# Kernel tuning notes

Hardware: AMD Instinct MI355X
Metric: run time of the kernel (lower is better)

The kernel has to match this reference:

```python
import jax, jax.numpy as jnp
import numpy as np

B, T, N, F_IN, H, E, L = 4, 12, 10000, 16, 64, 160000, 2


def setup_inputs() -> dict:
    key = jax.random.key(0)
    ks = jax.random.split(key, 10)
    s = 0.05  # small init scale for stability
    return {
        "x": jax.random.normal(ks[0], (B, T, N, F_IN), jnp.float32),
        "edge_index": jax.random.randint(ks[1], (2, E), 0, N, dtype=jnp.int32),
        "edge_weight": jax.random.uniform(ks[2], (E,), jnp.float32),
        "W_pre": jax.random.normal(ks[3], (F_IN, H), jnp.float32) * s,
        "b_pre": jnp.zeros((H,), jnp.float32),
        "W_lin": jax.random.normal(ks[4], (L, H, H), jnp.float32) * s,
        "W_root": jax.random.normal(ks[5], (L, H, H), jnp.float32) * s,
        "b_conv": jnp.zeros((L, H), jnp.float32),
        "W_ih": jax.random.normal(ks[6], (3 * H, H), jnp.float32) * s,
        "W_hh": jax.random.normal(ks[7], (3 * H, H), jnp.float32) * s,
        "b_ih": jnp.zeros((3 * H,), jnp.float32),
        "b_hh": jnp.zeros((3 * H,), jnp.float32),
    }


def reference(x, edge_index, edge_weight, W_pre, b_pre, W_lin, W_root, b_conv,
              W_ih, W_hh, b_ih, b_hh):
    b, t, n, _ = x.shape
    hdim = W_pre.shape[1]

    # preprocess: LazyLinear + ReLU, then fold time into batch: (b*t, n, h)
    h = jax.nn.relu(x @ W_pre + b_pre).reshape(b * t, n, hdim)

    # symmetric edge normalization (GCN-style): w_ij / sqrt(deg_i * deg_j)
    src, dst = edge_index[0], edge_index[1]
    deg = jnp.zeros((n,), h.dtype).at[dst].add(edge_weight)
    dinv = jnp.where(deg > 0, jax.lax.rsqrt(jnp.where(deg > 0, deg, 1.0)), 0.0)
    w = dinv[src] * edge_weight * dinv[dst]  # [E]

    # stacked GraphConv layers: gather -> weight -> scatter-add + root + bias, ReLU
    for l in range(W_lin.shape[0]):
        m = h @ W_lin[l]                                   # [BT, N, H]
        msg = m[:, src, :] * w[None, :, None]              # [BT, E, H] gather
        agg = jnp.zeros_like(m).at[:, dst, :].add(msg)     # scatter-add
        h = jax.nn.relu(agg + h @ W_root[l] + b_conv[l])

    # (b, t, n, h) -> (b*n, t, h) sequences for the GRU
    seq = h.reshape(b, t, n, hdim).transpose(0, 2, 1, 3).reshape(b * n, t, hdim)

    def gru_step(hprev, xt):
        gi = xt @ W_ih.T + b_ih
        gh = hprev @ W_hh.T + b_hh
        i_r, i_z, i_n = jnp.split(gi, 3, axis=-1)
        h_r, h_z, h_n = jnp.split(gh, 3, axis=-1)
        r = jax.nn.sigmoid(i_r + h_r)
        z = jax.nn.sigmoid(i_z + h_z)
        ng = jnp.tanh(i_n + r * h_n)
        hnew = (1.0 - z) * ng + z * hprev
        return hnew, None

    h0 = jnp.zeros((b * n, hdim), h.dtype)
    hlast, _ = jax.lax.scan(gru_step, h0, seq.transpose(1, 0, 2))  # carry = last output
    return hlast.reshape(b, n, hdim)
```

## Files before the change

### kernel.cpp

```cpp
#include <hip/hip_runtime.h>
#include <cstdint>
#include <cstddef>

#define B_ 4
#define T_ 12
#define N_ 10000
#define FIN_ 16
#define H_ 64
#define E_ 160000
#define BT_ (B_*T_)
#define ROWS_ (BT_*N_)
#define GRU_ROWS_ (B_*N_)
#define PAD_ 68

__device__ __forceinline__ float sigmoidf_(float x){ return 1.0f/(1.0f + __expf(-x)); }
__device__ __forceinline__ float tanhf_(float x){
  float ax = fabsf(x);
  float e  = __expf(-2.0f*ax);
  float t  = (1.0f - e)/(1.0f + e);
  return copysignf(t, x);
}

__global__ __launch_bounds__(256) void k_pre(const float* __restrict__ x,
    const float* __restrict__ Wp, const float* __restrict__ bp,
    float* __restrict__ A){
  __shared__ float sW[FIN_*H_];
  __shared__ float sb[H_];
  for (int i = threadIdx.x; i < FIN_*H_; i += 256) sW[i] = Wp[i];
  if (threadIdx.x < H_) sb[threadIdx.x] = bp[threadIdx.x];
  __syncthreads();
  int r = blockIdx.x*256 + threadIdx.x;
  if (r >= ROWS_) return;
  int bt = r / N_;
  int n  = r - bt*N_;
  const float4* xr = reinterpret_cast<const float4*>(x + (size_t)r*FIN_);
  float4 xv[4];
  #pragma unroll
  for (int i=0;i<4;i++) xv[i] = xr[i];
  const float* xk = reinterpret_cast<const float*>(xv);
  float4 acc[16];
  #pragma unroll
  for (int j=0;j<16;j++) acc[j] = reinterpret_cast<const float4*>(sb)[j];
  #pragma unroll
  for (int k=0;k<16;k++){
    float a = xk[k];
    const float4* wr = reinterpret_cast<const float4*>(sW + k*H_);
    #pragma unroll
    for (int j=0;j<16;j++){
      float4 w = wr[j];
      acc[j].x = fmaf(a, w.x, acc[j].x);
      acc[j].y = fmaf(a, w.y, acc[j].y);
      acc[j].z = fmaf(a, w.z, acc[j].z);
      acc[j].w = fmaf(a, w.w, acc[j].w);
    }
  }
  float4* outp = reinterpret_cast<float4*>(A + ((size_t)n*BT_ + bt)*H_);
  #pragma unroll
  for (int j=0;j<16;j++){
    float4 o = acc[j];
    o.x = fmaxf(o.x, 0.f); o.y = fmaxf(o.y, 0.f);
    o.z = fmaxf(o.z, 0.f); o.w = fmaxf(o.w, 0.f);
    outp[j] = o;
  }
}

__global__ void k_deg(const int* __restrict__ ei, const float* __restrict__ ew,
                      float* __restrict__ wdeg, int* __restrict__ cnt){
  int e = blockIdx.x*256 + threadIdx.x;
  if (e >= E_) return;
  int d = ei[E_ + e];
  atomicAdd(&wdeg[d], ew[e]);
  atomicAdd(&cnt[d], 1);
}

__global__ __launch_bounds__(1024) void k_scan(const int* __restrict__ cnt,
                                               int* __restrict__ rs){
  __shared__ int sb[1024];
  int tid = threadIdx.x;
  int base = tid*10;
  int loc[10]; int s = 0;
  #pragma unroll
  for (int j=0;j<10;j++){
    loc[j] = s;
    int v = (base+j < N_) ? cnt[base+j] : 0;
    s += v;
  }
  sb[tid] = s;
  __syncthreads();
  for (int off=1; off<1024; off<<=1){
    int v = (tid >= off) ? sb[tid-off] : 0;
    __syncthreads();
    sb[tid] += v;
    __syncthreads();
  }
  int pre = (tid>0) ? sb[tid-1] : 0;
  #pragma unroll
  for (int j=0;j<10;j++){
    if (base+j <= N_) rs[base+j] = pre + loc[j];
  }
}

__global__ void k_dinv(const float* __restrict__ wdeg, float* __restrict__ dinv){
  int i = blockIdx.x*256 + threadIdx.x;
  if (i >= N_) return;
  float dg = wdeg[i];
  dinv[i] = (dg > 0.f) ? rsqrtf(dg) : 0.f;
}

__global__ void k_fill(const int* __restrict__ ei, const float* __restrict__ ew,
                       const float* __restrict__ dinv, const int* __restrict__ rs,
                       int* __restrict__ fillc, int* __restrict__ src_s,
                       float* __restrict__ w_s){
  int e = blockIdx.x*256 + threadIdx.x;
  if (e >= E_) return;
  int s = ei[e], d = ei[E_ + e];
  float wn = dinv[s]*ew[e]*dinv[d];
  int slot = rs[d] + atomicAdd(&fillc[d], 1);
  src_s[slot] = s;
  w_s[slot]  = wn;
}

__global__ __launch_bounds__(256) void k_agg(const float* __restrict__ Ain,
    float* __restrict__ Aout, const float* __restrict__ Wl,
    const float* __restrict__ Wr, const float* __restrict__ bc,
    const int* __restrict__ rs, const int* __restrict__ src_s,
    const float* __restrict__ w_s){
  __shared__ float As[BT_*PAD_];
  __shared__ float Gs[BT_*PAD_];
  int n = blockIdx.x;
  int tid = threadIdx.x;
  const float4* Ain4 = reinterpret_cast<const float4*>(Ain + (size_t)n*BT_*H_);
  #pragma unroll
  for (int j=0;j<3;j++){
    int i = tid + j*256;
    int bt = i >> 4, c4 = i & 15;
    *reinterpret_cast<float4*>(As + bt*PAD_ + c4*4) = Ain4[i];
  }
  int wv = tid >> 6, L = tid & 63;
  int start = rs[n], end = rs[n+1];
  float4 acc[3];
  #pragma unroll
  for (int j=0;j<3;j++) acc[j] = make_float4(0.f,0.f,0.f,0.f);
  int e = start;
  for (; e+3 < end; e += 4){
    int   s0=src_s[e], s1=src_s[e+1], s2=src_s[e+2], s3=src_s[e+3];
    float w0=w_s[e],  w1=w_s[e+1],  w2=w_s[e+2],  w3=w_s[e+3];
    const float4* p0 = reinterpret_cast<const float4*>(Ain) + (size_t)s0*768 + wv*192 + L;
    const float4* p1 = reinterpret_cast<const float4*>(Ain) + (size_t)s1*768 + wv*192 + L;
    const float4* p2 = reinterpret_cast<const float4*>(Ain) + (size_t)s2*768 + wv*192 + L;
    const float4* p3 = reinterpret_cast<const float4*>(Ain) + (size_t)s3*768 + wv*192 + L;
    float4 v0[3], v1[3], v2[3], v3[3];
    #pragma unroll
    for (int j=0;j<3;j++){ v0[j]=p0[j*64]; v1[j]=p1[j*64]; v2[j]=p2[j*64]; v3[j]=p3[j*64]; }
    #pragma unroll
    for (int j=0;j<3;j++){
      acc[j].x = fmaf(w0, v0[j].x, acc[j].x); acc[j].y = fmaf(w0, v0[j].y, acc[j].y);
      acc[j].z = fmaf(w0, v0[j].z, acc[j].z); acc[j].w = fmaf(w0, v0[j].w, acc[j].w);
      acc[j].x = fmaf(w1, v1[j].x, acc[j].x); acc[j].y = fmaf(w1, v1[j].y, acc[j].y);
      acc[j].z = fmaf(w1, v1[j].z, acc[j].z); acc[j].w = fmaf(w1, v1[j].w, acc[j].w);
      acc[j].x = fmaf(w2, v2[j].x, acc[j].x); acc[j].y = fmaf(w2, v2[j].y, acc[j].y);
      acc[j].z = fmaf(w2, v2[j].z, acc[j].z); acc[j].w = fmaf(w2, v2[j].w, acc[j].w);
      acc[j].x = fmaf(w3, v3[j].x, acc[j].x); acc[j].y = fmaf(w3, v3[j].y, acc[j].y);
      acc[j].z = fmaf(w3, v3[j].z, acc[j].z); acc[j].w = fmaf(w3, v3[j].w, acc[j].w);
    }
  }
  for (; e < end; ++e){
    int s0 = src_s[e]; float w0 = w_s[e];
    const float4* p0 = reinterpret_cast<const float4*>(Ain) + (size_t)s0*768 + wv*192 + L;
    #pragma unroll
    for (int j=0;j<3;j++){
      float4 v = p0[j*64];
      acc[j].x = fmaf(w0, v.x, acc[j].x); acc[j].y = fmaf(w0, v.y, acc[j].y);
      acc[j].z = fmaf(w0, v.z, acc[j].z); acc[j].w = fmaf(w0, v.w, acc[j].w);
    }
  }
  {
    int bt0 = wv*12 + (L>>4), c4 = (L&15)*4;
    #pragma unroll
    for (int j=0;j<3;j++)
      *reinterpret_cast<float4*>(Gs + (bt0 + j*4)*PAD_ + c4) = acc[j];
  }
  __syncthreads();
  int bt0 = wv*12 + (L>>4);
  int c4  = (L&15)*4;
  float4 bv = *reinterpret_cast<const float4*>(bc + c4);
  float4 out[3];
  #pragma unroll
  for (int j=0;j<3;j++) out[j] = bv;
  #pragma unroll 2
  for (int k4=0;k4<16;k4++){
    float4 wl[4], wr[4];
    #pragma unroll
    for (int i=0;i<4;i++){
      wl[i] = *reinterpret_cast<const float4*>(Wl + (k4*4+i)*H_ + c4);
      wr[i] = *reinterpret_cast<const float4*>(Wr + (k4*4+i)*H_ + c4);
    }
    #pragma unroll
    for (int j=0;j<3;j++){
      float4 g4 = *reinterpret_cast<const float4*>(Gs + (bt0 + j*4)*PAD_ + k4*4);
      float4 a4 = *reinterpret_cast<const float4*>(As + (bt0 + j*4)*PAD_ + k4*4);
      out[j].x = fmaf(g4.x, wl[0].x, out[j].x); out[j].y = fmaf(g4.x, wl[0].y, out[j].y);
      out[j].z = fmaf(g4.x, wl[0].z, out[j].z); out[j].w = fmaf(g4.x, wl[0].w, out[j].w);
      out[j].x = fmaf(g4.y, wl[1].x, out[j].x); out[j].y = fmaf(g4.y, wl[1].y, out[j].y);
      out[j].z = fmaf(g4.y, wl[1].z, out[j].z); out[j].w = fmaf(g4.y, wl[1].w, out[j].w);
      out[j].x = fmaf(g4.z, wl[2].x, out[j].x); out[j].y = fmaf(g4.z, wl[2].y, out[j].y);
      out[j].z = fmaf(g4.z, wl[2].z, out[j].z); out[j].w = fmaf(g4.z, wl[2].w, out[j].w);
      out[j].x = fmaf(g4.w, wl[3].x, out[j].x); out[j].y = fmaf(g4.w, wl[3].y, out[j].y);
      out[j].z = fmaf(g4.w, wl[3].z, out[j].z); out[j].w = fmaf(g4.w, wl[3].w, out[j].w);
      out[j].x = fmaf(a4.x, wr[0].x, out[j].x); out[j].y = fmaf(a4.x, wr[0].y, out[j].y);
      out[j].z = fmaf(a4.x, wr[0].z, out[j].z); out[j].w = fmaf(a4.x, wr[0].w, out[j].w);
      out[j].x = fmaf(a4.y, wr[1].x, out[j].x); out[j].y = fmaf(a4.y, wr[1].y, out[j].y);
      out[j].z = fmaf(a4.y, wr[1].z, out[j].z); out[j].w = fmaf(a4.y, wr[1].w, out[j].w);
      out[j].x = fmaf(a4.z, wr[2].x, out[j].x); out[j].y = fmaf(a4.z, wr[2].y, out[j].y);
      out[j].z = fmaf(a4.z, wr[2].z, out[j].z); out[j].w = fmaf(a4.z, wr[2].w, out[j].w);
      out[j].x = fmaf(a4.w, wr[3].x, out[j].x); out[j].y = fmaf(a4.w, wr[3].y, out[j].y);
      out[j].z = fmaf(a4.w, wr[3].z, out[j].z); out[j].w = fmaf(a4.w, wr[3].w, out[j].w);
    }
  }
  float4* Aout4 = reinterpret_cast<float4*>(Aout + (size_t)n*BT_*H_);
  #pragma unroll
  for (int j=0;j<3;j++){
    float4 o = out[j];
    o.x = fmaxf(o.x, 0.f); o.y = fmaxf(o.y, 0.f);
    o.z = fmaxf(o.z, 0.f); o.w = fmaxf(o.w, 0.f);
    Aout4[wv*192 + j*64 + L] = o;
  }
}

__global__ __launch_bounds__(512) void k_gru(const float* __restrict__ A,
    const float* __restrict__ Wih, const float* __restrict__ Whh,
    const float* __restrict__ bih, const float* __restrict__ bhh,
    float* __restrict__ out){
  extern __shared__ float lds[];
  float* Wk = lds;
  int tid = threadIdx.x;
  int wv = tid >> 6;
  int lane = tid & 63;
  float* xs = lds + 24576 + wv*1024;
  float* hs = xs + 512;
  #pragma unroll
  for (int j=0;j<12;j++){
    int i = tid + j*512;
    int g = i >> 4, c4 = i & 15;
    int s = g >> 6, o = g & 63;
    float4 v = (g < 192)
      ? *reinterpret_cast<const float4*>(Wih + g*H_ + c4*4)
      : *reinterpret_cast<const float4*>(Whh + (g-192)*H_ + c4*4);
    *reinterpret_cast<float4*>(Wk + s*4096 + c4*256 + o*4) = v;
  }
  __syncthreads();
  float hreg[8];
  #pragma unroll
  for (int r=0;r<8;r++){ hreg[r] = 0.f; hs[r*64 + lane] = 0.f; }

  const float* wbi = Wk + lane*4;
  const float* wbh = Wk + 12288 + lane*4;

  int row0 = blockIdx.x*64 + wv*8;
  int bb = row0 / N_;
  int nn0 = row0 - bb*N_;
  float b0 = bih[lane]        + bhh[lane];
  float b1 = bih[64 + lane]   + bhh[64 + lane];
  float b2i = bih[128 + lane];
  float b2h = bhh[128 + lane];
  int xr0 = lane >> 4, xc4 = lane & 15;
  int xr1 = 4 + xr0;
  const float* Abase0 = A + ((size_t)(nn0 + xr0)*BT_ + bb*T_)*H_;
  const float* Abase1 = A + ((size_t)(nn0 + xr1)*BT_ + bb*T_)*H_;

  float4 xv0 = *reinterpret_cast<const float4*>(Abase0 + xc4*4);
  float4 xv1 = *reinterpret_cast<const float4*>(Abase1 + xc4*4);
  #pragma unroll 1
  for (int t=0; t<T_; t++){
    *reinterpret_cast<float4*>(xs + xr0*64 + xc4*4) = xv0;
    *reinterpret_cast<float4*>(xs + xr1*64 + xc4*4) = xv1;
    int tn = (t < T_-1) ? t+1 : t;
    float4 xv0n = *reinterpret_cast<const float4*>(Abase0 + (size_t)tn*H_ + xc4*4);
    float4 xv1n = *reinterpret_cast<const float4*>(Abase1 + (size_t)tn*H_ + xc4*4);

    float ar[8], az[8], ani[8], anh[8];
    #pragma unroll
    for (int r=0;r<8;r++){ ar[r] = b0; az[r] = b1; ani[r] = b2i; anh[r] = b2h; }

    #pragma unroll 4
    for (int k4=0;k4<16;k4++){
      float4 wi0 = *reinterpret_cast<const float4*>(wbi + k4*256);
      float4 wi1 = *reinterpret_cast<const float4*>(wbi + 4096 + k4*256);
      float4 wi2 = *reinterpret_cast<const float4*>(wbi + 8192 + k4*256);
      float4 wh0 = *reinterpret_cast<const float4*>(wbh + k4*256);
      float4 wh1 = *reinterpret_cast<const float4*>(wbh + 4096 + k4*256);
      float4 wh2 = *reinterpret_cast<const float4*>(wbh + 8192 + k4*256);
      #pragma unroll
      for (int r=0;r<8;r++){
        float4 xw = *reinterpret_cast<const float4*>(xs + r*64 + k4*4);
        float4 hw = *reinterpret_cast<const float4*>(hs + r*64 + k4*4);
        ar[r] = fmaf(wi0.x, xw.x, ar[r]);  ar[r] = fmaf(wh0.x, hw.x, ar[r]);
        ar[r] = fmaf(wi0.y, xw.y, ar[r]);  ar[r] = fmaf(wh0.y, hw.y, ar[r]);
        ar[r] = fmaf(wi0.z, xw.z, ar[r]);  ar[r] = fmaf(wh0.z, hw.z, ar[r]);
        ar[r] = fmaf(wi0.w, xw.w, ar[r]);  ar[r] = fmaf(wh0.w, hw.w, ar[r]);
        az[r] = fmaf(wi1.x, xw.x, az[r]);  az[r] = fmaf(wh1.x, hw.x, az[r]);
        az[r] = fmaf(wi1.y, xw.y, az[r]);  az[r] = fmaf(wh1.y, hw.y, az[r]);
        az[r] = fmaf(wi1.z, xw.z, az[r]);  az[r] = fmaf(wh1.z, hw.z, az[r]);
        az[r] = fmaf(wi1.w, xw.w, az[r]);  az[r] = fmaf(wh1.w, hw.w, az[r]);
        ani[r] = fmaf(wi2.x, xw.x, ani[r]);
        ani[r] = fmaf(wi2.y, xw.y, ani[r]);
        ani[r] = fmaf(wi2.z, xw.z, ani[r]);
        ani[r] = fmaf(wi2.w, xw.w, ani[r]);
        anh[r] = fmaf(wh2.x, hw.x, anh[r]);
        anh[r] = fmaf(wh2.y, hw.y, anh[r]);
        anh[r] = fmaf(wh2.z, hw.z, anh[r]);
        anh[r] = fmaf(wh2.w, hw.w, anh[r]);
      }
    }
    #pragma unroll
    for (int r=0;r<8;r++){
      float rr = sigmoidf_(ar[r]);
      float zz = sigmoidf_(az[r]);
      float ng = tanhf_(ani[r] + rr*anh[r]);
      float hn = (1.f - zz)*ng + zz*hreg[r];
      hreg[r] = hn;
      hs[r*64 + lane] = hn;
    }
    xv0 = xv0n; xv1 = xv1n;
  }
  #pragma unroll
  for (int r=0;r<8;r++)
    out[(size_t)(row0 + r)*H_ + lane] = hreg[r];
}

extern "C" void kernel_launch(void* const* d_in, const int* in_sizes, int n_in,
                              void* d_out, int out_size, void* d_ws, size_t ws_size,
                              hipStream_t stream){
  const float* x     = (const float*)d_in[0];
  const int*   ei    = (const int*)d_in[1];
  const float* ew    = (const float*)d_in[2];
  const float* Wpre  = (const float*)d_in[3];
  const float* bpre  = (const float*)d_in[4];
  const float* Wlin  = (const float*)d_in[5];
  const float* Wroot = (const float*)d_in[6];
  const float* bconv = (const float*)d_in[7];
  const float* Wih   = (const float*)d_in[8];
  const float* Whh   = (const float*)d_in[9];
  const float* bih   = (const float*)d_in[10];
  const float* bhh   = (const float*)d_in[11];
  float* out = (float*)d_out;

  float* ws   = (float*)d_ws;
  float* A0   = ws;
  float* A1   = A0 + (size_t)ROWS_*H_;
  float* wdeg = A1 + (size_t)ROWS_*H_;
  float* dinv = wdeg + N_;
  float* w_s  = dinv + N_;
  int*   cnt   = (int*)(w_s + E_);
  int*   fillc = cnt + N_;
  int*   rs    = fillc + N_;
  int*   src_s = rs + (N_+1);

  hipMemsetAsync(wdeg, 0, N_*sizeof(float), stream);
  hipMemsetAsync(cnt,  0, 2*N_*sizeof(int), stream);

  k_pre<<<ROWS_/256, 256, 0, stream>>>(x, Wpre, bpre, A0);
  k_deg<<<E_/256, 256, 0, stream>>>(ei, ew, wdeg, cnt);
  k_scan<<<1, 1024, 0, stream>>>(cnt, rs);
  k_dinv<<<(N_+255)/256, 256, 0, stream>>>(wdeg, dinv);
  k_fill<<<E_/256, 256, 0, stream>>>(ei, ew, dinv, rs, fillc, src_s, w_s);

  k_agg<<<N_, 256, 0, stream>>>(A0, A1, Wlin,         Wroot,         bconv,
                                rs, src_s, w_s);
  k_agg<<<N_, 256, 0, stream>>>(A1, A0, Wlin + H_*H_, Wroot + H_*H_, bconv + H_,
                                rs, src_s, w_s);

  hipFuncSetAttribute((const void*)k_gru,
      hipFuncAttributeMaxDynamicSharedMemorySize, 131072);
  k_gru<<<GRU_ROWS_/64, 512, 131072, stream>>>(A0, Wih, Whh, bih, bhh, out);
}
```

Before: 1.178 ms.

## Broadcast GRU inputs and hidden state via readlane instead of LDS

The GRU kernel no longer stages the per-row input and hidden vectors in LDS. Each lane keeps its column of x and h in registers, and the scalars needed for the matvec are taken with readlane broadcasts. This removes the LDS stores and reloads on every timestep and cuts dynamic shared memory from 128KB to 96KB, which may allow more blocks per CU. In exchange, each readlane with an unrolled index adds scalar instructions and register pressure, and the x loads become scalar-per-lane rather than float4.

```diff
diff --git a/kernel.cpp b/kernel.cpp
--- a/kernel.cpp
+++ b/kernel.cpp
@@ -19,6 +19,9 @@
   float e  = __expf(-2.0f*ax);
   float t  = (1.0f - e)/(1.0f + e);
   return copysignf(t, x);
+}
+__device__ __forceinline__ float rdl_(float v, int k){
+  return __int_as_float(__builtin_amdgcn_readlane(__float_as_int(v), k));
 }
 
 __global__ __launch_bounds__(256) void k_pre(const float* __restrict__ x,
@@ -236,8 +239,6 @@
   int tid = threadIdx.x;
   int wv = tid >> 6;
   int lane = tid & 63;
-  float* xs = lds + 24576 + wv*1024;
-  float* hs = xs + 512;
   #pragma unroll
   for (int j=0;j<12;j++){
     int i = tid + j*512;
@@ -249,9 +250,6 @@
     *reinterpret_cast<float4*>(Wk + s*4096 + c4*256 + o*4) = v;
   }
   __syncthreads();
-  float hreg[8];
-  #pragma unroll
-  for (int r=0;r<8;r++){ hreg[r] = 0.f; hs[r*64 + lane] = 0.f; }
 
   const float* wbi = Wk + lane*4;
   const float* wbh = Wk + 12288 + lane*4;
@@ -259,30 +257,31 @@
   int row0 = blockIdx.x*64 + wv*8;
   int bb = row0 / N_;
   int nn0 = row0 - bb*N_;
-  float b0 = bih[lane]        + bhh[lane];
-  float b1 = bih[64 + lane]   + bhh[64 + lane];
+  float b0  = bih[lane]      + bhh[lane];
+  float b1  = bih[64 + lane] + bhh[64 + lane];
   float b2i = bih[128 + lane];
   float b2h = bhh[128 + lane];
-  int xr0 = lane >> 4, xc4 = lane & 15;
-  int xr1 = 4 + xr0;
-  const float* Abase0 = A + ((size_t)(nn0 + xr0)*BT_ + bb*T_)*H_;
-  const float* Abase1 = A + ((size_t)(nn0 + xr1)*BT_ + bb*T_)*H_;
-
-  float4 xv0 = *reinterpret_cast<const float4*>(Abase0 + xc4*4);
-  float4 xv1 = *reinterpret_cast<const float4*>(Abase1 + xc4*4);
+
+  float hreg[8], xcur[8];
+  #pragma unroll
+  for (int r=0;r<8;r++){
+    hreg[r] = 0.f;
+    xcur[r] = A[((size_t)(nn0 + r)*BT_ + bb*T_)*H_ + lane];
+  }
+
   #pragma unroll 1
   for (int t=0; t<T_; t++){
-    *reinterpret_cast<float4*>(xs + xr0*64 + xc4*4) = xv0;
-    *reinterpret_cast<float4*>(xs + xr1*64 + xc4*4) = xv1;
+    float xnxt[8];
     int tn = (t < T_-1) ? t+1 : t;
-    float4 xv0n = *reinterpret_cast<const float4*>(Abase0 + (size_t)tn*H_ + xc4*4);
-    float4 xv1n = *reinterpret_cast<const float4*>(Abase1 + (size_t)tn*H_ + xc4*4);
+    #pragma unroll
+    for (int r=0;r<8;r++)
+      xnxt[r] = A[((size_t)(nn0 + r)*BT_ + bb*T_ + tn)*H_ + lane];
 
     float ar[8], az[8], ani[8], anh[8];
     #pragma unroll
-    for (int r=0;r<8;r++){ ar[r] = b0; az[r] = b1; ani[r] = b2i; anh[r] = b2h; }
-
-    #pragma unroll 4
+    for (int r=0;r<8;r++){ ar[r]=b0; az[r]=b1; ani[r]=b2i; anh[r]=b2h; }
+
+    #pragma unroll 2
     for (int k4=0;k4<16;k4++){
       float4 wi0 = *reinterpret_cast<const float4*>(wbi + k4*256);
       float4 wi1 = *reinterpret_cast<const float4*>(wbi + 4096 + k4*256);
@@ -290,26 +289,26 @@
       float4 wh0 = *reinterpret_cast<const float4*>(wbh + k4*256);
       float4 wh1 = *reinterpret_cast<const float4*>(wbh + 4096 + k4*256);
       float4 wh2 = *reinterpret_cast<const float4*>(wbh + 8192 + k4*256);
+      const float* i0 = reinterpret_cast<const float*>(&wi0);
+      const float* i1 = reinterpret_cast<const float*>(&wi1);
+      const float* i2 = reinterpret_cast<const float*>(&wi2);
+      const float* h0 = reinterpret_cast<const float*>(&wh0);
+      const float* h1 = reinterpret_cast<const float*>(&wh1);
+      const float* h2 = reinterpret_cast<const float*>(&wh2);
       #pragma unroll
       for (int r=0;r<8;r++){
-        float4 xw = *reinterpret_cast<const float4*>(xs + r*64 + k4*4);
-        float4 hw = *reinterpret_cast<const float4*>(hs + r*64 + k4*4);
-        ar[r] = fmaf(wi0.x, xw.x, ar[r]);  ar[r] = fmaf(wh0.x, hw.x, ar[r]);
-        ar[r] = fmaf(wi0.y, xw.y, ar[r]);  ar[r] = fmaf(wh0.y, hw.y, ar[r]);
-        ar[r] = fmaf(wi0.z, xw.z, ar[r]);  ar[r] = fmaf(wh0.z, hw.z, ar[r]);
-        ar[r] = fmaf(wi0.w, xw.w, ar[r]);  ar[r] = fmaf(wh0.w, hw.w, ar[r]);
-        az[r] = fmaf(wi1.x, xw.x, az[r]);  az[r] = fmaf(wh1.x, hw.x, az[r]);
-        az[r] = fmaf(wi1.y, xw.y, az[r]);  az[r] = fmaf(wh1.y, hw.y, az[r]);
-        az[r] = fmaf(wi1.z, xw.z, az[r]);  az[r] = fmaf(wh1.z, hw.z, az[r]);
-        az[r] = fmaf(wi1.w, xw.w, az[r]);  az[r] = fmaf(wh1.w, hw.w, az[r]);
-        ani[r] = fmaf(wi2.x, xw.x, ani[r]);
-        ani[r] = fmaf(wi2.y, xw.y, ani[r]);
-        ani[r] = fmaf(wi2.z, xw.z, ani[r]);
-        ani[r] = fmaf(wi2.w, xw.w, ani[r]);
-        anh[r] = fmaf(wh2.x, hw.x, anh[r]);
-        anh[r] = fmaf(wh2.y, hw.y, anh[r]);
-        anh[r] = fmaf(wh2.z, hw.z, anh[r]);
-        anh[r] = fmaf(wh2.w, hw.w, anh[r]);
+        #pragma unroll
+        for (int i=0;i<4;i++){
+          int k = k4*4 + i;
+          float xsc = rdl_(xcur[r], k);
+          float hsc = rdl_(hreg[r], k);
+          ar[r]  = fmaf(i0[i], xsc, ar[r]);
+          ar[r]  = fmaf(h0[i], hsc, ar[r]);
+          az[r]  = fmaf(i1[i], xsc, az[r]);
+          az[r]  = fmaf(h1[i], hsc, az[r]);
+          ani[r] = fmaf(i2[i], xsc, ani[r]);
+          anh[r] = fmaf(h2[i], hsc, anh[r]);
+        }
       }
     }
     #pragma unroll
@@ -317,11 +316,9 @@
       float rr = sigmoidf_(ar[r]);
       float zz = sigmoidf_(az[r]);
       float ng = tanhf_(ani[r] + rr*anh[r]);
-      float hn = (1.f - zz)*ng + zz*hreg[r];
-      hreg[r] = hn;
-      hs[r*64 + lane] = hn;
-    }
-    xv0 = xv0n; xv1 = xv1n;
+      hreg[r] = (1.f - zz)*ng + zz*hreg[r];
+      xcur[r] = xnxt[r];
+    }
   }
   #pragma unroll
   for (int r=0;r<8;r++)
@@ -371,6 +368,6 @@
                                 rs, src_s, w_s);
 
   hipFuncSetAttribute((const void*)k_gru,
-      hipFuncAttributeMaxDynamicSharedMemorySize, 131072);
-  k_gru<<<GRU_ROWS_/64, 512, 131072, stream>>>(A0, Wih, Whh, bih, bhh, out);
-}
+      hipFuncAttributeMaxDynamicSharedMemorySize, 98304);
+  k_gru<<<GRU_ROWS_/64, 512, 98304, stream>>>(A0, Wih, Whh, bih, bhh, out);
+}
```

Result: slower. 1.267 ms (+7.5%).
